# Performance work log

Measured on AMD Instinct MI355X. Metric: run time of the kernel, lower is better.

The kernel has to match this reference:

```python
import jax, jax.numpy as jnp
import numpy as np

N, S, EMB, H = 4, 2048, 512, 8
D = EMB // H  # 64


def setup_inputs() -> dict:
    key = jax.random.key(0)
    ks = jax.random.split(key, 10)
    sc = 0.02
    return {
        "x": jax.random.normal(ks[0], (N, S, EMB), dtype=jnp.float32),
        "Wq": jax.random.normal(ks[1], (D, D), dtype=jnp.float32) * sc,
        "bq": jax.random.normal(ks[2], (D,), dtype=jnp.float32) * sc,
        "Wk": jax.random.normal(ks[3], (D, D), dtype=jnp.float32) * sc,
        "bk": jax.random.normal(ks[4], (D,), dtype=jnp.float32) * sc,
        "Wv": jax.random.normal(ks[5], (D, D), dtype=jnp.float32) * sc,
        "bv": jax.random.normal(ks[6], (D,), dtype=jnp.float32) * sc,
        "E": jax.random.normal(ks[7], (1, S, D), dtype=jnp.float32),
        "Wo": jax.random.normal(ks[8], (EMB, EMB), dtype=jnp.float32) * sc,
        "bo": jax.random.normal(ks[9], (EMB,), dtype=jnp.float32) * sc,
    }


def reference(x, Wq, bq, Wk, bk, Wv, bv, E, Wo, bo):
    n, s, emb = x.shape
    h, d = H, D
    xh = x.reshape(n, s, h, d)
    # per-head Linear projections (torch Linear: y = x @ W.T + b)
    q = xh @ Wq.T + bq  # [n,s,h,d]
    k = xh @ Wk.T + bk
    v = xh @ Wv.T + bv

    # QE = queries.transpose(1,2) @ E.transpose(1,2) -> [n,h,s,s]
    QE = jnp.einsum('nqhd,sd->nhqs', q, E[0])
    # _mask_positions: zero where triu(ones(S,S),1) flipped along columns == 1
    triu1 = jnp.triu(jnp.ones((s, s), dtype=bool), 1)
    QE = jnp.where(triu1[:, ::-1], 0.0, QE)
    # _skew: pad last dim on the left, reinterpret (s, s+1) as (s+1, s), drop first row
    padded = jnp.pad(QE, ((0, 0), (0, 0), (0, 0), (1, 0)))  # [n,h,s,s+1]
    Smat = padded.reshape(n, h, s + 1, s)[:, :, 1:, :]  # [n,h,s,s]

    qk = jnp.einsum('nqhd,nkhd->nhqk', q, k)
    # faithful to source: fill where mask==0 (lower triangle incl. diag) with -1e20
    qk = jnp.where(triu1, qk, jnp.float32(-1e20))
    attention = jax.nn.softmax(qk / (emb ** 0.5), axis=3) + Smat

    z = jnp.einsum('nhql,nlhd->nqhd', attention, v).reshape(n, s, h * d)
    return z @ Wo.T + bo


if __name__ == "__main__":
    out = reference(**setup_inputs())
    print(out.shape, out.dtype)
```

## Files before the change

kernel.cpp:

```cpp
#include <hip/hip_runtime.h>
#include <hip/hip_bf16.h>

#define S_LEN 2048
#define EMB   512
#define NH    8
#define DH    64
#define NB    4

typedef float f32x4  __attribute__((ext_vector_type(4)));
typedef short short8 __attribute__((ext_vector_type(8)));

__device__ __forceinline__ unsigned short f2bf_rn(float f) {
    return __builtin_bit_cast(unsigned short, __float2bfloat16(f));
}

__device__ __forceinline__ f32x4 mfma16(short8 a, short8 b, f32x4 c) {
    return __builtin_amdgcn_mfma_f32_16x16x32_bf16(a, b, c, 0, 0, 0);
}

__device__ __forceinline__ short8 frag_read(const unsigned short* lds, int row, int oct)
{
    const char* src = (const char*)lds + row * 128 + ((oct * 16) ^ ((row & 7) << 4));
    return *reinterpret_cast<const short8*>(src);
}

__device__ __forceinline__ int pinv(int k) {
    return (k & 32) + ((k >> 2) & 3) * 8 + (k & 3) + ((k & 16) >> 2);
}

__device__ __forceinline__ void stage_tile_f32(const float* __restrict__ g,
                                               int gstride, unsigned short* lds, int tid)
{
    #pragma unroll
    for (int c = tid; c < 512; c += 256) {
        const int r = c >> 3, s = c & 7;
        const float4* src = (const float4*)(g + (size_t)r * gstride + s * 8);
        const float4 a = src[0], b = src[1];
        short8 f;
        f[0] = (short)f2bf_rn(a.x); f[1] = (short)f2bf_rn(a.y);
        f[2] = (short)f2bf_rn(a.z); f[3] = (short)f2bf_rn(a.w);
        f[4] = (short)f2bf_rn(b.x); f[5] = (short)f2bf_rn(b.y);
        f[6] = (short)f2bf_rn(b.z); f[7] = (short)f2bf_rn(b.w);
        char* dst = (char*)lds + r * 128 + ((s * 16) ^ ((r & 7) << 4));
        *reinterpret_cast<short8*>(dst) = f;
    }
}

__device__ __forceinline__ void softmax_pack(const f32x4 C[4], bool diag, int ws, int og,
                                             int rowg, float& dsum, short8& pa0, short8& pa1)
{
    constexpr float SM_SCALE = 0.04419417382415922f;
    float rs[4];
    unsigned short pw[16];
    if (!diag) {
        #pragma unroll
        for (int t = 0; t < 4; ++t) {
            float a = 0.f;
            #pragma unroll
            for (int r = 0; r < 4; ++r) {
                const float wv = __expf(C[t][r] * SM_SCALE);
                a += wv;
                pw[t * 4 + r] = f2bf_rn(wv);
            }
            rs[t] = a;
        }
    } else {
        #pragma unroll
        for (int t = 0; t < 4; ++t) {
            float a = 0.f;
            #pragma unroll
            for (int r = 0; r < 4; ++r) {
                const bool keep = (t > ws) || (t == ws && (og * 4 + r) > rowg);
                const float wv = keep ? __expf(C[t][r] * SM_SCALE) : 0.f;
                a += wv;
                pw[t * 4 + r] = f2bf_rn(wv);
            }
            rs[t] = a;
        }
    }
    dsum += (rs[0] + rs[1]) + (rs[2] + rs[3]);
    #pragma unroll
    for (int i = 0; i < 8; ++i) { pa0[i] = (short)pw[i]; pa1[i] = (short)pw[8 + i]; }
}

__global__ __launch_bounds__(256) void qkv_mfma(
    const float* __restrict__ x,
    const float* __restrict__ Wq, const float* __restrict__ bq,
    const float* __restrict__ Wk, const float* __restrict__ bk,
    const float* __restrict__ Wv, const float* __restrict__ bv,
    unsigned short* __restrict__ qg, unsigned short* __restrict__ kg,
    unsigned short* __restrict__ vg)
{
    __shared__ unsigned short w_lds[3][64 * 64];

    const int tid  = threadIdx.x;
    const int lane = tid & 63;
    const int w    = tid >> 6;
    const int rowg = lane & 15;
    const int og   = lane >> 4;

    stage_tile_f32(Wq, 64, w_lds[0], tid);
    stage_tile_f32(Wk, 64, w_lds[1], tid);
    stage_tile_f32(Wv, 64, w_lds[2], tid);

    float bias[3][4];
    #pragma unroll
    for (int t = 0; t < 4; ++t) {
        bias[0][t] = bq[16 * t + rowg];
        bias[1][t] = bk[16 * t + rowg];
        bias[2][t] = bv[16 * t + rowg];
    }

    const int m0 = blockIdx.x * 64 + 16 * w;
    const float* xr = x + (size_t)(m0 + rowg) * 64;
    const float4 a0 = *(const float4*)(xr + og * 8);
    const float4 a1 = *(const float4*)(xr + og * 8 + 4);
    const float4 a2 = *(const float4*)(xr + 32 + og * 8);
    const float4 a3 = *(const float4*)(xr + 32 + og * 8 + 4);
    short8 af0, af1;
    af0[0] = (short)f2bf_rn(a0.x); af0[1] = (short)f2bf_rn(a0.y);
    af0[2] = (short)f2bf_rn(a0.z); af0[3] = (short)f2bf_rn(a0.w);
    af0[4] = (short)f2bf_rn(a1.x); af0[5] = (short)f2bf_rn(a1.y);
    af0[6] = (short)f2bf_rn(a1.z); af0[7] = (short)f2bf_rn(a1.w);
    af1[0] = (short)f2bf_rn(a2.x); af1[1] = (short)f2bf_rn(a2.y);
    af1[2] = (short)f2bf_rn(a2.z); af1[3] = (short)f2bf_rn(a2.w);
    af1[4] = (short)f2bf_rn(a3.x); af1[5] = (short)f2bf_rn(a3.y);
    af1[6] = (short)f2bf_rn(a3.z); af1[7] = (short)f2bf_rn(a3.w);

    __syncthreads();

    f32x4 acc[3][4];
    #pragma unroll
    for (int m = 0; m < 3; ++m)
        #pragma unroll
        for (int t = 0; t < 4; ++t) {
            const float b = bias[m][t];
            acc[m][t] = (f32x4){b, b, b, b};
        }

    #pragma unroll
    for (int m = 0; m < 3; ++m)
        #pragma unroll
        for (int t = 0; t < 4; ++t) {
            acc[m][t] = mfma16(af0, frag_read(w_lds[m], 16 * t + rowg, og),     acc[m][t]);
            acc[m][t] = mfma16(af1, frag_read(w_lds[m], 16 * t + rowg, og + 4), acc[m][t]);
        }

    unsigned short* outp[3] = {qg, kg, vg};
    #pragma unroll
    for (int m = 0; m < 3; ++m)
        #pragma unroll
        for (int r = 0; r < 4; ++r) {
            const int mr = (blockIdx.x * 64 + 16 * w) + og * 4 + r;
            const int tk = mr >> 3, h = mr & 7;
            const int n = tk >> 11, s = tk & 2047;
            const size_t rowb = (((size_t)(n * NH + h)) * S_LEN + s) * 64;
            #pragma unroll
            for (int t = 0; t < 4; ++t)
                outp[m][rowb + 16 * t + rowg] = f2bf_rn(acc[m][t][r]);
        }
}

__global__ __launch_bounds__(256) void transpose_v(
    const unsigned short* __restrict__ v, unsigned short* __restrict__ vt)
{
    __shared__ unsigned short t_lds[64][72];
    const int bid = blockIdx.x;
    const int st = bid % (S_LEN / 64);
    const int nh = bid / (S_LEN / 64);
    const unsigned short* vp = v + ((size_t)nh * S_LEN + st * 64) * DH;
    unsigned short* vtp = vt + (size_t)nh * DH * S_LEN + st * 64;
    const int tid = threadIdx.x;
    #pragma unroll
    for (int c = tid; c < 512; c += 256) {
        const int r = c >> 3, s = c & 7;
        short8 xv = *reinterpret_cast<const short8*>(vp + r * DH + s * 8);
        #pragma unroll
        for (int i = 0; i < 8; ++i) t_lds[s * 8 + i][r] = (unsigned short)xv[i];
    }
    __syncthreads();
    #pragma unroll
    for (int c = tid; c < 512; c += 256) {
        const int d = c >> 3, sc = c & 7;
        const int cb = ((sc & 4) << 3) + (sc & 3) * 4;
        short8 y;
        #pragma unroll
        for (int i = 0; i < 8; ++i)
            y[i] = (short)t_lds[d][cb + (i & 3) + ((i & 4) << 2)];
        *reinterpret_cast<short8*>(vtp + (size_t)d * S_LEN + sc * 8) = y;
    }
}

__global__ __launch_bounds__(256) void prep_e(
    const float* __restrict__ E, unsigned short* __restrict__ eb)
{
    const int i = blockIdx.x * 256 + threadIdx.x;
    if (i >= S_LEN * DH) return;
    const int dlt = i >> 6, d = i & 63;
    eb[i] = f2bf_rn(E[(size_t)(S_LEN - 1 - dlt) * DH + d]);
}

__global__ __launch_bounds__(256) void attn_mfma(
    const unsigned short* __restrict__ qg,
    const unsigned short* __restrict__ kg,
    const unsigned short* __restrict__ vtg,
    const unsigned short* __restrict__ eg,
    unsigned short* __restrict__ z)
{
    __shared__ __align__(16) unsigned short smem[20480];

    constexpr float UNI = 1.0f / 2048.0f;

    const int nqt = S_LEN / 64;
    const int bid = blockIdx.x;
    const int qt  = (nqt - 1) - (bid >> 5);
    const int nh  = bid & 31;
    const int q0  = qt * 64;
    const size_t base = (size_t)nh * S_LEN * DH;
    const unsigned short* qp = qg + base;
    const unsigned short* kp = kg + base;
    const unsigned short* vp = vtg + base;

    const int tid  = threadIdx.x;
    const int lane = tid & 63;
    const int w    = tid >> 6;
    const int rowg = lane & 15;
    const int og   = lane >> 4;

    const int r0 = tid >> 3,  s0 = tid & 7;
    const int r1 = r0 + 32;
    const int ldsoff0 = r0 * 128 + ((s0 * 16) ^ ((r0 & 7) << 4));
    const int ldsoff1 = r1 * 128 + ((s0 * 16) ^ ((r1 & 7) << 4));
    const int ksrc0 = r0 * 64 + s0 * 8,    ksrc1 = r1 * 64 + s0 * 8;
    const int vsrc0 = r0 * S_LEN + s0 * 8, vsrc1 = r1 * S_LEN + s0 * 8;

    short8 kr0, kr1, vr0, vr1;

    short8 qa0, qa1;
    {
        const unsigned short* qr = qp + (size_t)(q0 + 16 * w + rowg) * DH + og * 8;
        qa0 = *reinterpret_cast<const short8*>(qr);
        qa1 = *reinterpret_cast<const short8*>(qr + 32);
    }

    const f32x4 zero4 = {0.f, 0.f, 0.f, 0.f};
    f32x4 accS[4], accR[4];
    #pragma unroll
    for (int t = 0; t < 4; ++t) { accS[t] = zero4; accR[t] = zero4; }
    float dsum = 0.f;

    const int T = (S_LEN - q0) >> 6;
    kr0 = *(const short8*)(kp + (size_t)q0 * 64 + ksrc0);
    kr1 = *(const short8*)(kp + (size_t)q0 * 64 + ksrc1);
    vr0 = *(const short8*)(vp + q0 + vsrc0);
    vr1 = *(const short8*)(vp + q0 + vsrc1);
    *(short8*)((char*)smem + ldsoff0) = kr0;
    *(short8*)((char*)smem + ldsoff1) = kr1;
    *(short8*)((char*)(smem + 8192) + ldsoff0) = vr0;
    *(short8*)((char*)(smem + 8192) + ldsoff1) = vr1;
    __syncthreads();

    short8 pa0, pa1;
    for (int ti = 0; ti < T; ++ti) {
        const bool pf = (ti + 1 < T);
        if (pf) {
            const unsigned short* kb = kp + (size_t)(q0 + (ti + 1) * 64) * 64;
            const unsigned short* vb = vp + (q0 + (ti + 1) * 64);
            kr0 = *(const short8*)(kb + ksrc0);
            kr1 = *(const short8*)(kb + ksrc1);
            vr0 = *(const short8*)(vb + vsrc0);
            vr1 = *(const short8*)(vb + vsrc1);
        }
        const unsigned short* klds = smem + (ti & 1) * 4096;

        __builtin_amdgcn_s_setprio(1);
        f32x4 C[4];
        #pragma unroll
        for (int t = 0; t < 4; ++t) {
            const short8 kf0 = frag_read(klds, 16 * t + rowg, og);
            const short8 kf1 = frag_read(klds, 16 * t + rowg, og + 4);
            C[t] = mfma16(kf1, qa1, mfma16(kf0, qa0, zero4));
        }
        if (ti > 0) {
            const unsigned short* vprev = smem + 8192 + ((ti + 2) % 3) * 4096;
            #pragma unroll
            for (int tt = 0; tt < 4; ++tt) {
                const short8 vf0 = frag_read(vprev, 16 * tt + rowg, og);
                const short8 vf1 = frag_read(vprev, 16 * tt + rowg, og + 4);
                accS[tt] = mfma16(pa1, vf1, mfma16(pa0, vf0, accS[tt]));
            }
        }
        __builtin_amdgcn_s_setprio(0);

        if (pf) {
            unsigned short* kn = smem + ((ti + 1) & 1) * 4096;
            unsigned short* vn = smem + 8192 + ((ti + 1) % 3) * 4096;
            *(short8*)((char*)kn + ldsoff0) = kr0;
            *(short8*)((char*)kn + ldsoff1) = kr1;
            *(short8*)((char*)vn + ldsoff0) = vr0;
            *(short8*)((char*)vn + ldsoff1) = vr1;
        }
        softmax_pack(C, ti == 0, w, og, rowg, dsum, pa0, pa1);
        __syncthreads();
    }
    {
        const unsigned short* vprev = smem + 8192 + ((T + 2) % 3) * 4096;
        __builtin_amdgcn_s_setprio(1);
        #pragma unroll
        for (int tt = 0; tt < 4; ++tt) {
            const short8 vf0 = frag_read(vprev, 16 * tt + rowg, og);
            const short8 vf1 = frag_read(vprev, 16 * tt + rowg, og + 4);
            accS[tt] = mfma16(pa1, vf1, mfma16(pa0, vf0, accS[tt]));
        }
        __builtin_amdgcn_s_setprio(0);
    }
    __syncthreads();

    unsigned short* const ebuf = smem + 16384;
    const int jmax = q0 >> 6;

    kr0 = *(const short8*)(eg + ksrc0);
    kr1 = *(const short8*)(eg + ksrc1);
    vr0 = *(const short8*)(vp + q0 + vsrc0);
    vr1 = *(const short8*)(vp + q0 + vsrc1);
    {
        const short8 z8 = {0, 0, 0, 0, 0, 0, 0, 0};
        #pragma unroll
        for (int c2 = 0; c2 < 2; ++c2) {
            const int cc = lane + 64 * c2;
            const int r = 16 * w + (cc >> 3), sc = cc & 7;
            *reinterpret_cast<short8*>((char*)smem + r * 128 + sc * 16) = z8;
        }
    }
    *(short8*)((char*)ebuf + ldsoff0) = kr0;
    *(short8*)((char*)ebuf + ldsoff1) = kr1;
    *(short8*)((char*)(smem + 8192) + ldsoff0) = vr0;
    *(short8*)((char*)(smem + 8192) + ldsoff1) = vr1;
    __syncthreads();

    for (int j = 0; j <= jmax; ++j) {
        const bool pf = (j < jmax);
        if (pf) {
            const unsigned short* ebn = eg + (size_t)(j + 1) * 4096;
            const unsigned short* vbn = vp + (q0 - 64 * (j + 1));
            kr0 = *(const short8*)(ebn + ksrc0);
            kr1 = *(const short8*)(ebn + ksrc1);
            vr0 = *(const short8*)(vbn + vsrc0);
            vr1 = *(const short8*)(vbn + vsrc1);
        }
        const unsigned short* vlds = smem + 8192 + (j & 1) * 4096;

        __builtin_amdgcn_s_setprio(1);
        f32x4 G[4];
        #pragma unroll
        for (int t = 0; t < 4; ++t)
            G[t] = mfma16(qa1, frag_read(ebuf, 16 * t + rowg, og + 4),
                   mfma16(qa0, frag_read(ebuf, 16 * t + rowg, og), zero4));
        __builtin_amdgcn_s_setprio(0);

        unsigned short* pc = smem + (j & 1) * 4096;
        unsigned short* pn = smem + ((j + 1) & 1) * 4096;
        #pragma unroll
        for (int t = 0; t < 4; ++t) {
            const int c = 16 * t + rowg;
            #pragma unroll
            for (int r = 0; r < 4; ++r) {
                const int qq = 16 * w + og * 4 + r;
                float val = G[t][r];
                if (q0 + qq == S_LEN - 1) val += UNI;
                const unsigned short bv = f2bf_rn(val);
                const int swz = (qq & 7) << 4;
                if (c <= qq) {
                    const int p = pinv(qq - c);
                    *(unsigned short*)((char*)pc + qq * 128 + ((p * 2) ^ swz)) = bv;
                } else if (pf) {
                    const int p = pinv(qq - c + 64);
                    *(unsigned short*)((char*)pn + qq * 128 + ((p * 2) ^ swz)) = bv;
                }
            }
        }

        const short8 pb0 = frag_read(pc, 16 * w + rowg, og);
        const short8 pb1 = frag_read(pc, 16 * w + rowg, og + 4);
        __builtin_amdgcn_s_setprio(1);
        #pragma unroll
        for (int tt = 0; tt < 4; ++tt) {
            const short8 vf0 = frag_read(vlds, 16 * tt + rowg, og);
            const short8 vf1 = frag_read(vlds, 16 * tt + rowg, og + 4);
            accR[tt] = mfma16(pb1, vf1, mfma16(pb0, vf0, accR[tt]));
        }
        __builtin_amdgcn_s_setprio(0);

        __syncthreads();
        if (pf) {
            unsigned short* vn = smem + 8192 + ((j + 1) & 1) * 4096;
            *(short8*)((char*)ebuf + ldsoff0) = kr0;
            *(short8*)((char*)ebuf + ldsoff1) = kr1;
            *(short8*)((char*)vn + ldsoff0) = vr0;
            *(short8*)((char*)vn + ldsoff1) = vr1;
            __syncthreads();
        }
    }

    dsum += __shfl_xor(dsum, 16);
    dsum += __shfl_xor(dsum, 32);

    const int n = nh >> 3, h = nh & 7;
    const int qrow0 = q0 + 16 * w + og * 4;
    #pragma unroll
    for (int r = 0; r < 4; ++r) {
        const int qrow = qrow0 + r;
        const float dn = __shfl(dsum, og * 4 + r);
        const float inv = (qrow == S_LEN - 1) ? 0.f : 1.f / dn;
        #pragma unroll
        for (int t = 0; t < 4; ++t) {
            const float zv = accS[t][r] * inv + accR[t][r];
            z[((size_t)n * S_LEN + qrow) * EMB + h * DH + 16 * t + rowg] = f2bf_rn(zv);
        }
    }
}

__global__ __launch_bounds__(256) void outproj_mfma(
    const unsigned short* __restrict__ z,
    const float* __restrict__ Wo, const float* __restrict__ bo,
    float* __restrict__ out)
{
    __shared__ unsigned short wo_lds[64 * 64];

    const int tid  = threadIdx.x;
    const int lane = tid & 63;
    const int w    = tid >> 6;
    const int rowg = lane & 15;
    const int og   = lane >> 4;

    const int nob = EMB / 64;
    const int mb = blockIdx.x / nob;
    const int ob = blockIdx.x % nob;
    const int m0 = mb * 64 + 16 * w;
    const int o0 = ob * 64;

    f32x4 acc[4];
    #pragma unroll
    for (int t = 0; t < 4; ++t) {
        const float b = bo[o0 + 16 * t + rowg];
        acc[t] = (f32x4){b, b, b, b};
    }

    for (int k0 = 0; k0 < EMB; k0 += 64) {
        __syncthreads();
        stage_tile_f32(Wo + (size_t)o0 * EMB + k0, EMB, wo_lds, tid);
        __syncthreads();
        const unsigned short* zr = z + (size_t)(m0 + rowg) * EMB + k0;
        const short8 af0 = *reinterpret_cast<const short8*>(zr + og * 8);
        const short8 af1 = *reinterpret_cast<const short8*>(zr + 32 + og * 8);
        #pragma unroll
        for (int t = 0; t < 4; ++t) {
            acc[t] = mfma16(af0, frag_read(wo_lds, 16 * t + rowg, og),     acc[t]);
            acc[t] = mfma16(af1, frag_read(wo_lds, 16 * t + rowg, og + 4), acc[t]);
        }
    }

    #pragma unroll
    for (int r = 0; r < 4; ++r) {
        const size_t rowb = (size_t)(m0 + og * 4 + r) * EMB + o0;
        #pragma unroll
        for (int t = 0; t < 4; ++t)
            out[rowb + 16 * t + rowg] = acc[t][r];
    }
}

extern "C" void kernel_launch(void* const* d_in, const int* in_sizes, int n_in,
                              void* d_out, int out_size, void* d_ws, size_t ws_size,
                              hipStream_t stream) {
    const float* x  = (const float*)d_in[0];
    const float* Wq = (const float*)d_in[1];
    const float* bq = (const float*)d_in[2];
    const float* Wk = (const float*)d_in[3];
    const float* bk = (const float*)d_in[4];
    const float* Wv = (const float*)d_in[5];
    const float* bv = (const float*)d_in[6];
    const float* E  = (const float*)d_in[7];
    const float* Wo = (const float*)d_in[8];
    const float* bo = (const float*)d_in[9];
    float* out = (float*)d_out;

    const size_t per = (size_t)NB * NH * S_LEN * DH;
    unsigned short* qb  = (unsigned short*)d_ws;
    unsigned short* kb  = qb  + per;
    unsigned short* vb  = kb  + per;
    unsigned short* vtb = vb  + per;
    unsigned short* eb  = vtb + per;
    unsigned short* zb  = eb + (size_t)S_LEN * DH;

    qkv_mfma<<<(NB * S_LEN * NH) / 64, 256, 0, stream>>>(x, Wq, bq, Wk, bk, Wv, bv,
                                                         qb, kb, vb);
    transpose_v<<<NB * NH * (S_LEN / 64), 256, 0, stream>>>(vb, vtb);
    prep_e<<<(S_LEN * DH + 255) / 256, 256, 0, stream>>>(E, eb);
    attn_mfma<<<NB * NH * (S_LEN / 64), 256, 0, stream>>>(qb, kb, vtb, eb, zb);
    outproj_mfma<<<(NB * S_LEN / 64) * (EMB / 64), 256, 0, stream>>>(zb, Wo, bo, out);
}
```

Measured before the change: 102.5 us.

## Split softmax phase by key columns per wave, reduce partial PV through LDS

```diff
diff --git a/kernel.cpp b/kernel.cpp
--- a/kernel.cpp
+++ b/kernel.cpp
@@ -9,6 +9,7 @@
 
 typedef float f32x4  __attribute__((ext_vector_type(4)));
 typedef short short8 __attribute__((ext_vector_type(8)));
+typedef short short4v __attribute__((ext_vector_type(4)));
 
 __device__ __forceinline__ unsigned short f2bf_rn(float f) {
     return __builtin_bit_cast(unsigned short, __float2bfloat16(f));
@@ -18,10 +19,29 @@
     return __builtin_amdgcn_mfma_f32_16x16x32_bf16(a, b, c, 0, 0, 0);
 }
 
+__device__ __forceinline__ f32x4 mfma16h(short4v a, short4v b, f32x4 c) {
+#if __has_builtin(__builtin_amdgcn_mfma_f32_16x16x16bf16_1k)
+    return __builtin_amdgcn_mfma_f32_16x16x16bf16_1k(a, b, c, 0, 0, 0);
+#elif __has_builtin(__builtin_amdgcn_mfma_f32_16x16x16_bf16)
+    return __builtin_amdgcn_mfma_f32_16x16x16_bf16(a, b, c, 0, 0, 0);
+#else
+    f32x4 d = c;
+    asm volatile("s_nop 1\n\tv_mfma_f32_16x16x16_bf16 %0, %1, %2, %0\n\ts_nop 7\n\ts_nop 2"
+                 : "+v"(d) : "v"(a), "v"(b));
+    return d;
+#endif
+}
+
 __device__ __forceinline__ short8 frag_read(const unsigned short* lds, int row, int oct)
 {
     const char* src = (const char*)lds + row * 128 + ((oct * 16) ^ ((row & 7) << 4));
     return *reinterpret_cast<const short8*>(src);
+}
+
+__device__ __forceinline__ short4v frag_read64(const unsigned short* lds, int row, int colbyte)
+{
+    const char* src = (const char*)lds + row * 128 + (colbyte ^ ((row & 7) << 4));
+    return *reinterpret_cast<const short4v*>(src);
 }
 
 __device__ __forceinline__ int pinv(int k) {
@@ -44,43 +64,6 @@
         char* dst = (char*)lds + r * 128 + ((s * 16) ^ ((r & 7) << 4));
         *reinterpret_cast<short8*>(dst) = f;
     }
-}
-
-__device__ __forceinline__ void softmax_pack(const f32x4 C[4], bool diag, int ws, int og,
-                                             int rowg, float& dsum, short8& pa0, short8& pa1)
-{
-    constexpr float SM_SCALE = 0.04419417382415922f;
-    float rs[4];
-    unsigned short pw[16];
-    if (!diag) {
-        #pragma unroll
-        for (int t = 0; t < 4; ++t) {
-            float a = 0.f;
-            #pragma unroll
-            for (int r = 0; r < 4; ++r) {
-                const float wv = __expf(C[t][r] * SM_SCALE);
-                a += wv;
-                pw[t * 4 + r] = f2bf_rn(wv);
-            }
-            rs[t] = a;
-        }
-    } else {
-        #pragma unroll
-        for (int t = 0; t < 4; ++t) {
-            float a = 0.f;
-            #pragma unroll
-            for (int r = 0; r < 4; ++r) {
-                const bool keep = (t > ws) || (t == ws && (og * 4 + r) > rowg);
-                const float wv = keep ? __expf(C[t][r] * SM_SCALE) : 0.f;
-                a += wv;
-                pw[t * 4 + r] = f2bf_rn(wv);
-            }
-            rs[t] = a;
-        }
-    }
-    dsum += (rs[0] + rs[1]) + (rs[2] + rs[3]);
-    #pragma unroll
-    for (int i = 0; i < 8; ++i) { pa0[i] = (short)pw[i]; pa1[i] = (short)pw[8 + i]; }
 }
 
 __global__ __launch_bounds__(256) void qkv_mfma(
@@ -209,6 +192,7 @@
 {
     __shared__ __align__(16) unsigned short smem[20480];
 
+    constexpr float SM_SCALE = 0.04419417382415922f;
     constexpr float UNI = 1.0f / 2048.0f;
 
     const int nqt = S_LEN / 64;
@@ -236,18 +220,23 @@
 
     short8 kr0, kr1, vr0, vr1;
 
-    short8 qa0, qa1;
-    {
-        const unsigned short* qr = qp + (size_t)(q0 + 16 * w + rowg) * DH + og * 8;
-        qa0 = *reinterpret_cast<const short8*>(qr);
-        qa1 = *reinterpret_cast<const short8*>(qr + 32);
-    }
+    short8 qa[4][2];
+    #pragma unroll
+    for (int t = 0; t < 4; ++t) {
+        const unsigned short* qr = qp + (size_t)(q0 + 16 * t + rowg) * DH + og * 8;
+        qa[t][0] = *reinterpret_cast<const short8*>(qr);
+        qa[t][1] = *reinterpret_cast<const short8*>(qr + 32);
+    }
+    const int vcolb = pinv(16 * w + 4 * og) * 2;
 
     const f32x4 zero4 = {0.f, 0.f, 0.f, 0.f};
-    f32x4 accS[4], accR[4];
-    #pragma unroll
-    for (int t = 0; t < 4; ++t) { accS[t] = zero4; accR[t] = zero4; }
-    float dsum = 0.f;
+    f32x4 acc2[4][4];
+    #pragma unroll
+    for (int u = 0; u < 4; ++u)
+        #pragma unroll
+        for (int t = 0; t < 4; ++t) acc2[u][t] = zero4;
+    float dsv[4] = {0.f, 0.f, 0.f, 0.f};
+    short4v pb[4];
 
     const int T = (S_LEN - q0) >> 6;
     kr0 = *(const short8*)(kp + (size_t)q0 * 64 + ksrc0);
@@ -260,7 +249,6 @@
     *(short8*)((char*)(smem + 8192) + ldsoff1) = vr1;
     __syncthreads();
 
-    short8 pa0, pa1;
     for (int ti = 0; ti < T; ++ti) {
         const bool pf = (ti + 1 < T);
         if (pf) {
@@ -274,21 +262,22 @@
         const unsigned short* klds = smem + (ti & 1) * 4096;
 
         __builtin_amdgcn_s_setprio(1);
+        const short8 kf0 = frag_read(klds, 16 * w + rowg, og);
+        const short8 kf1 = frag_read(klds, 16 * w + rowg, og + 4);
         f32x4 C[4];
         #pragma unroll
-        for (int t = 0; t < 4; ++t) {
-            const short8 kf0 = frag_read(klds, 16 * t + rowg, og);
-            const short8 kf1 = frag_read(klds, 16 * t + rowg, og + 4);
-            C[t] = mfma16(kf1, qa1, mfma16(kf0, qa0, zero4));
-        }
+        for (int t = 0; t < 4; ++t)
+            C[t] = mfma16(kf1, qa[t][1], mfma16(kf0, qa[t][0], zero4));
         if (ti > 0) {
             const unsigned short* vprev = smem + 8192 + ((ti + 2) % 3) * 4096;
-            #pragma unroll
-            for (int tt = 0; tt < 4; ++tt) {
-                const short8 vf0 = frag_read(vprev, 16 * tt + rowg, og);
-                const short8 vf1 = frag_read(vprev, 16 * tt + rowg, og + 4);
-                accS[tt] = mfma16(pa1, vf1, mfma16(pa0, vf0, accS[tt]));
-            }
+            short4v va[4];
+            #pragma unroll
+            for (int u = 0; u < 4; ++u) va[u] = frag_read64(vprev, 16 * u + rowg, vcolb);
+            #pragma unroll
+            for (int u = 0; u < 4; ++u)
+                #pragma unroll
+                for (int t = 0; t < 4; ++t)
+                    acc2[u][t] = mfma16h(va[u], pb[t], acc2[u][t]);
         }
         __builtin_amdgcn_s_setprio(0);
 
@@ -300,29 +289,111 @@
             *(short8*)((char*)vn + ldsoff0) = vr0;
             *(short8*)((char*)vn + ldsoff1) = vr1;
         }
-        softmax_pack(C, ti == 0, w, og, rowg, dsum, pa0, pa1);
+
+        {
+            const bool diag = (ti == 0);
+            #pragma unroll
+            for (int t = 0; t < 4; ++t) {
+                unsigned short pw[4];
+                float a0 = 0.f;
+                #pragma unroll
+                for (int r = 0; r < 4; ++r) {
+                    const bool keep = !diag || (w > t) || (w == t && og * 4 + r > rowg);
+                    const float wv = keep ? __expf(C[t][r] * SM_SCALE) : 0.f;
+                    a0 += wv;
+                    pw[r] = f2bf_rn(wv);
+                }
+                dsv[t] += a0;
+                short4v pbt = {(short)pw[0], (short)pw[1], (short)pw[2], (short)pw[3]};
+                pb[t] = pbt;
+            }
+        }
         __syncthreads();
     }
     {
         const unsigned short* vprev = smem + 8192 + ((T + 2) % 3) * 4096;
         __builtin_amdgcn_s_setprio(1);
+        short4v va[4];
+        #pragma unroll
+        for (int u = 0; u < 4; ++u) va[u] = frag_read64(vprev, 16 * u + rowg, vcolb);
+        #pragma unroll
+        for (int u = 0; u < 4; ++u)
+            #pragma unroll
+            for (int t = 0; t < 4; ++t)
+                acc2[u][t] = mfma16h(va[u], pb[t], acc2[u][t]);
+        __builtin_amdgcn_s_setprio(0);
+    }
+    __syncthreads();
+
+    #pragma unroll
+    for (int t = 0; t < 4; ++t) {
+        float v = dsv[t];
+        v += __shfl_xor(v, 16);
+        v += __shfl_xor(v, 32);
+        dsv[t] = v;
+    }
+    float* const dnb  = (float*)((char*)smem + 32768);
+    float* const bufA = (float*)smem;
+    float* const bufB = (float*)((char*)smem + 16384);
+    if (lane < 16) {
+        #pragma unroll
+        for (int t = 0; t < 4; ++t) dnb[w * 64 + 16 * t + lane] = dsv[t];
+    }
+    const short8 er0 = *(const short8*)(eg + ksrc0);
+    const short8 er1 = *(const short8*)(eg + ksrc1);
+    const short8 wr0 = *(const short8*)(vp + q0 + vsrc0);
+    const short8 wr1 = *(const short8*)(vp + q0 + vsrc1);
+    if (w < 2) {
+        float* buf = (w == 0) ? bufA : bufB;
+        #pragma unroll
+        for (int t = 0; t < 4; ++t) {
+            const int q = 16 * t + rowg;
+            char* rowb = (char*)buf + q * 256;
+            const int sw = (q & 7) << 4;
+            #pragma unroll
+            for (int u = 0; u < 4; ++u)
+                *(f32x4*)(rowb + (((4 * u + og) * 16) ^ sw)) = acc2[u][t];
+        }
+    }
+    __syncthreads();
+    if (w >= 2) {
+        float* buf = (w == 2) ? bufA : bufB;
+        #pragma unroll
+        for (int t = 0; t < 4; ++t) {
+            const int q = 16 * t + rowg;
+            char* rowb = (char*)buf + q * 256;
+            const int sw = (q & 7) << 4;
+            #pragma unroll
+            for (int u = 0; u < 4; ++u) {
+                f32x4* p = (f32x4*)(rowb + (((4 * u + og) * 16) ^ sw));
+                *p = *p + acc2[u][t];
+            }
+        }
+    }
+    __syncthreads();
+    f32x4 accS[4];
+    float dn[4];
+    #pragma unroll
+    for (int r = 0; r < 4; ++r) {
+        const int q = 16 * w + og * 4 + r;
+        dn[r] = (dnb[q] + dnb[64 + q]) + (dnb[128 + q] + dnb[192 + q]);
+        const int sw = (q & 7) << 4;
         #pragma unroll
         for (int tt = 0; tt < 4; ++tt) {
-            const short8 vf0 = frag_read(vprev, 16 * tt + rowg, og);
-            const short8 vf1 = frag_read(vprev, 16 * tt + rowg, og + 4);
-            accS[tt] = mfma16(pa1, vf1, mfma16(pa0, vf0, accS[tt]));
-        }
-        __builtin_amdgcn_s_setprio(0);
+            const int d = 16 * tt + rowg;
+            const int off = q * 256 + (((d >> 2) * 16) ^ sw) + (d & 3) * 4;
+            accS[tt][r] = *(const float*)((char*)bufA + off)
+                        + *(const float*)((char*)bufB + off);
+        }
     }
     __syncthreads();
 
     unsigned short* const ebuf = smem + 16384;
     const int jmax = q0 >> 6;
-
-    kr0 = *(const short8*)(eg + ksrc0);
-    kr1 = *(const short8*)(eg + ksrc1);
-    vr0 = *(const short8*)(vp + q0 + vsrc0);
-    vr1 = *(const short8*)(vp + q0 + vsrc1);
+    f32x4 accR[4];
+    #pragma unroll
+    for (int t = 0; t < 4; ++t) accR[t] = zero4;
+
     {
         const short8 z8 = {0, 0, 0, 0, 0, 0, 0, 0};
         #pragma unroll
@@ -332,10 +403,10 @@
             *reinterpret_cast<short8*>((char*)smem + r * 128 + sc * 16) = z8;
         }
     }
-    *(short8*)((char*)ebuf + ldsoff0) = kr0;
-    *(short8*)((char*)ebuf + ldsoff1) = kr1;
-    *(short8*)((char*)(smem + 8192) + ldsoff0) = vr0;
-    *(short8*)((char*)(smem + 8192) + ldsoff1) = vr1;
+    *(short8*)((char*)ebuf + ldsoff0) = er0;
+    *(short8*)((char*)ebuf + ldsoff1) = er1;
+    *(short8*)((char*)(smem + 8192) + ldsoff0) = wr0;
+    *(short8*)((char*)(smem + 8192) + ldsoff1) = wr1;
     __syncthreads();
 
     for (int j = 0; j <= jmax; ++j) {
@@ -354,8 +425,8 @@
         f32x4 G[4];
         #pragma unroll
         for (int t = 0; t < 4; ++t)
-            G[t] = mfma16(qa1, frag_read(ebuf, 16 * t + rowg, og + 4),
-                   mfma16(qa0, frag_read(ebuf, 16 * t + rowg, og), zero4));
+            G[t] = mfma16(qa[w][1], frag_read(ebuf, 16 * t + rowg, og + 4),
+                   mfma16(qa[w][0], frag_read(ebuf, 16 * t + rowg, og), zero4));
         __builtin_amdgcn_s_setprio(0);
 
         unsigned short* pc = smem + (j & 1) * 4096;
@@ -380,14 +451,14 @@
             }
         }
 
-        const short8 pb0 = frag_read(pc, 16 * w + rowg, og);
-        const short8 pb1 = frag_read(pc, 16 * w + rowg, og + 4);
+        const short8 sb0 = frag_read(pc, 16 * w + rowg, og);
+        const short8 sb1 = frag_read(pc, 16 * w + rowg, og + 4);
         __builtin_amdgcn_s_setprio(1);
         #pragma unroll
         for (int tt = 0; tt < 4; ++tt) {
             const short8 vf0 = frag_read(vlds, 16 * tt + rowg, og);
             const short8 vf1 = frag_read(vlds, 16 * tt + rowg, og + 4);
-            accR[tt] = mfma16(pb1, vf1, mfma16(pb0, vf0, accR[tt]));
+            accR[tt] = mfma16(sb1, vf1, mfma16(sb0, vf0, accR[tt]));
         }
         __builtin_amdgcn_s_setprio(0);
 
@@ -402,16 +473,12 @@
         }
     }
 
-    dsum += __shfl_xor(dsum, 16);
-    dsum += __shfl_xor(dsum, 32);
-
     const int n = nh >> 3, h = nh & 7;
     const int qrow0 = q0 + 16 * w + og * 4;
     #pragma unroll
     for (int r = 0; r < 4; ++r) {
         const int qrow = qrow0 + r;
-        const float dn = __shfl(dsum, og * 4 + r);
-        const float inv = (qrow == S_LEN - 1) ? 0.f : 1.f / dn;
+        const float inv = (qrow == S_LEN - 1) ? 0.f : 1.f / dn[r];
         #pragma unroll
         for (int t = 0; t < 4; ++t) {
             const float zv = accS[t][r] * inv + accR[t][r];
```

New measurement: 140.0 us. 1.37x slower.
